# Kernel optimization log

Measured on AMD Instinct MI355X. Metric: run time of the kernel, lower is better.

Reference implementation:

```python
import jax, jax.numpy as jnp
import numpy as np

N, D = 4096, 128
NUM_CLASS = 500000
NUM_SAMPLES = 32768


def setup_inputs() -> dict:
    key = jax.random.key(0)
    k_x, k_w, k_b, k_id = jax.random.split(key, 4)
    x = jax.random.normal(k_x, (N, D), dtype=jnp.float32)
    # params.weight init uniform(-0.05, 0.05) in original; use randn-scaled equivalent scale
    weight = jax.random.normal(k_w, (NUM_CLASS, D), dtype=jnp.float32) * 0.05
    bias = jax.random.normal(k_b, (NUM_CLASS, 1), dtype=jnp.float32) * 0.01
    # sample_ids: candidate classes returned by the LSH hash-table query (host-side
    # data structure); modeled here as a precomputed index set.
    sample_ids = jax.random.randint(k_id, (NUM_SAMPLES,), 0, NUM_CLASS, dtype=jnp.int64)
    return {"x": x, "weight": weight, "bias": bias, "sample_ids": sample_ids}


def reference(x, weight, bias, sample_ids):
    # gather sampled class embeddings + biases (F.embedding equivalent)
    sample_weights = weight[sample_ids]            # [S, D]
    sample_bias = bias[:, 0][sample_ids]           # [S]
    # small GEMM: [N, D] @ [D, S] + [S]
    sample_logits = jnp.einsum("nd,sd->ns", x, sample_weights) + sample_bias
    return (sample_logits, sample_ids)
```

## Files before the change

### kernel.cpp

```cpp
#include <hip/hip_runtime.h>

#define NROWS 4096
#define DIM   128
#define SCOLS 32768

typedef short bf16x8 __attribute__((ext_vector_type(8)));
typedef float f32x4  __attribute__((ext_vector_type(4)));

__device__ __forceinline__ unsigned short f2bf(float f) {
    unsigned int u = __builtin_bit_cast(unsigned int, f);
    u += 0x7fffu + ((u >> 16) & 1u);
    return (unsigned short)(u >> 16);
}

#define WCHUNKS (SCOLS * 16)
#define XCHUNKS (NROWS * 16)

__global__ __launch_bounds__(256) void prep_kernel(
    const float* __restrict__ x, const float* __restrict__ weight,
    const float* __restrict__ bias, const int* __restrict__ ids,
    float* __restrict__ out, unsigned short* __restrict__ w_ws,
    unsigned short* __restrict__ x_ws, float* __restrict__ bias_ws)
{
    int gid = blockIdx.x * 256 + threadIdx.x;
    if (gid < WCHUNKS) {
        int r = gid >> 4, c = gid & 15;
        int id = ids[r];
        const float4* src = (const float4*)(weight + (size_t)id * DIM);
        float4 v0 = src[2 * c], v1 = src[2 * c + 1];
        union { unsigned short u[8]; uint4 q; } b;
        b.u[0] = f2bf(v0.x); b.u[1] = f2bf(v0.y); b.u[2] = f2bf(v0.z); b.u[3] = f2bf(v0.w);
        b.u[4] = f2bf(v1.x); b.u[5] = f2bf(v1.y); b.u[6] = f2bf(v1.z); b.u[7] = f2bf(v1.w);
        *(uint4*)&w_ws[(size_t)r * DIM + (size_t)((c ^ (r & 15)) * 8)] = b.q;
    } else if (gid < WCHUNKS + XCHUNKS) {
        int g = gid - WCHUNKS;
        int r = g >> 4, c = g & 15;
        const float4* src = (const float4*)(x + (size_t)r * DIM);
        float4 v0 = src[2 * c], v1 = src[2 * c + 1];
        union { unsigned short u[8]; uint4 q; } b;
        b.u[0] = f2bf(v0.x); b.u[1] = f2bf(v0.y); b.u[2] = f2bf(v0.z); b.u[3] = f2bf(v0.w);
        b.u[4] = f2bf(v1.x); b.u[5] = f2bf(v1.y); b.u[6] = f2bf(v1.z); b.u[7] = f2bf(v1.w);
        *(uint4*)&x_ws[(size_t)r * DIM + (size_t)((c ^ (r & 15)) * 8)] = b.q;
    } else {
        int g = gid - (WCHUNKS + XCHUNKS);
        if (g < SCOLS) {
            int id = ids[g];
            bias_ws[g] = bias[id];
            out[(size_t)NROWS * SCOLS + g] = (float)id;
        }
    }
}

__global__ __launch_bounds__(256, 2) void lsh_gemm2(
    const unsigned short* __restrict__ w_ws,
    const unsigned short* __restrict__ x_ws,
    const float* __restrict__ bias_ws,
    float* __restrict__ out)
{
    __shared__ unsigned short lds_w[128 * 128];
    __shared__ unsigned short lds_x[128 * 128];

    const int t    = threadIdx.x;
    const int s0   = blockIdx.x * 128;
    const int n0   = blockIdx.y * 128;
    const int lane = t & 63;
    const int wave = t >> 6;

    const char* wsrc = (const char*)(w_ws + (size_t)s0 * DIM);
    const char* xsrc = (const char*)(x_ws + (size_t)n0 * DIM);

    #pragma unroll
    for (int j = 0; j < 8; ++j) {
        int boff = wave * 8192 + j * 1024;
        int goff = boff + lane * 16;
        __builtin_amdgcn_global_load_lds(
            (const __attribute__((address_space(1))) void*)(wsrc + goff),
            (__attribute__((address_space(3))) void*)((char*)lds_w + boff),
            16, 0, 0);
        __builtin_amdgcn_global_load_lds(
            (const __attribute__((address_space(1))) void*)(xsrc + goff),
            (__attribute__((address_space(3))) void*)((char*)lds_x + boff),
            16, 0, 0);
    }
    __syncthreads();

    const int lrow = lane & 15;
    const int quad = lane >> 4;
    const int wn   = (wave & 1) * 64;
    const int wsc  = (wave >> 1) * 64;

    f32x4 acc[4][4];
    #pragma unroll
    for (int a = 0; a < 4; ++a)
        #pragma unroll
        for (int b = 0; b < 4; ++b)
            acc[a][b] = (f32x4){0.f, 0.f, 0.f, 0.f};

    #pragma unroll
    for (int kk = 0; kk < 4; ++kk) {
        bf16x8 aw[4], bx[4];
        int cb = kk * 4 + quad;
        #pragma unroll
        for (int i = 0; i < 4; ++i) {
            int rw = wsc + i * 16 + lrow;
            int rn = wn  + i * 16 + lrow;
            aw[i] = *(const bf16x8*)&lds_w[rw * 128 + ((cb ^ lrow) * 8)];
            bx[i] = *(const bf16x8*)&lds_x[rn * 128 + ((cb ^ lrow) * 8)];
        }
        #pragma unroll
        for (int a = 0; a < 4; ++a)
            #pragma unroll
            for (int b = 0; b < 4; ++b)
                acc[a][b] = __builtin_amdgcn_mfma_f32_16x16x32_bf16(
                    aw[a], bx[b], acc[a][b], 0, 0, 0);
    }

    #pragma unroll
    for (int a = 0; a < 4; ++a) {
        int sL = wsc + a * 16 + quad * 4;
        f32x4 b4 = *(const f32x4*)&bias_ws[s0 + sL];
        #pragma unroll
        for (int b = 0; b < 4; ++b) {
            int n = n0 + wn + b * 16 + lrow;
            f32x4 v = acc[a][b] + b4;
            __builtin_nontemporal_store(v, (f32x4*)&out[(size_t)n * SCOLS + (s0 + sL)]);
        }
    }
}

__global__ __launch_bounds__(256, 2) void lsh_gemm(
    const float* __restrict__ x,
    const float* __restrict__ weight,
    const float* __restrict__ bias,
    const int*   __restrict__ ids,
    float*       __restrict__ out)
{
    __shared__ unsigned short lds_x[128 * 128];
    __shared__ unsigned short lds_w[128 * 128];

    const int t  = threadIdx.x;
    const int s0 = blockIdx.x * 128;
    const int n0 = blockIdx.y * 128;

    #pragma unroll
    for (int i = 0; i < 16; ++i) {
        int f   = t + i * 256;
        int row = f >> 5;
        int c4  = f & 31;
        float4 v = ((const float4*)(x + (size_t)(n0 + row) * DIM))[c4];
        ushort4 b;
        b.x = f2bf(v.x); b.y = f2bf(v.y); b.z = f2bf(v.z); b.w = f2bf(v.w);
        int sw = (c4 >> 1) ^ (row & 15);
        *(ushort4*)&lds_x[row * 128 + sw * 8 + (c4 & 1) * 4] = b;
    }
    #pragma unroll
    for (int i = 0; i < 16; ++i) {
        int f   = t + i * 256;
        int row = f >> 5;
        int c4  = f & 31;
        int id  = ids[s0 + row];
        float4 v = ((const float4*)(weight + (size_t)id * DIM))[c4];
        ushort4 b;
        b.x = f2bf(v.x); b.y = f2bf(v.y); b.z = f2bf(v.z); b.w = f2bf(v.w);
        int sw = (c4 >> 1) ^ (row & 15);
        *(ushort4*)&lds_w[row * 128 + sw * 8 + (c4 & 1) * 4] = b;
    }
    __syncthreads();

    const int lane = t & 63;
    const int wave = t >> 6;
    const int lrow = lane & 15;
    const int quad = lane >> 4;
    const int wm   = (wave & 1) * 64;
    const int wsc  = (wave >> 1) * 64;

    f32x4 acc[4][4];
    #pragma unroll
    for (int a = 0; a < 4; ++a)
        #pragma unroll
        for (int b = 0; b < 4; ++b)
            acc[a][b] = (f32x4){0.f, 0.f, 0.f, 0.f};

    #pragma unroll
    for (int kk = 0; kk < 4; ++kk) {
        bf16x8 af[4], bv[4];
        int cbase = kk * 4 + quad;
        #pragma unroll
        for (int i = 0; i < 4; ++i) {
            int rowa = wm  + i * 16 + lrow;
            int rowb = wsc + i * 16 + lrow;
            af[i] = *(const bf16x8*)&lds_x[rowa * 128 + (cbase ^ lrow) * 8];
            bv[i] = *(const bf16x8*)&lds_w[rowb * 128 + (cbase ^ lrow) * 8];
        }
        #pragma unroll
        for (int tm = 0; tm < 4; ++tm)
            #pragma unroll
            for (int ts = 0; ts < 4; ++ts)
                acc[tm][ts] = __builtin_amdgcn_mfma_f32_16x16x32_bf16(
                    af[tm], bv[ts], acc[tm][ts], 0, 0, 0);
    }

    #pragma unroll
    for (int ts = 0; ts < 4; ++ts) {
        int colL = wsc + ts * 16 + lrow;
        int col  = s0 + colL;
        float bvps = bias[ids[s0 + colL]];
        #pragma unroll
        for (int tm = 0; tm < 4; ++tm) {
            int rowbase = n0 + wm + tm * 16 + quad * 4;
            #pragma unroll
            for (int r = 0; r < 4; ++r)
                out[(size_t)(rowbase + r) * SCOLS + col] = acc[tm][ts][r] + bvps;
        }
    }
}

__global__ void ids_out_kernel(const int* __restrict__ ids, float* __restrict__ out)
{
    int i = blockIdx.x * 256 + threadIdx.x;
    if (i < SCOLS)
        out[(size_t)NROWS * SCOLS + i] = (float)ids[i];
}

extern "C" void kernel_launch(void* const* d_in, const int* in_sizes, int n_in,
                              void* d_out, int out_size, void* d_ws, size_t ws_size,
                              hipStream_t stream) {
    const float* x      = (const float*)d_in[0];
    const float* weight = (const float*)d_in[1];
    const float* bias   = (const float*)d_in[2];
    const int*   ids    = (const int*)d_in[3];
    float*       out    = (float*)d_out;

    const size_t W_BYTES = (size_t)SCOLS * DIM * 2;
    const size_t X_BYTES = (size_t)NROWS * DIM * 2;
    const size_t B_BYTES = (size_t)SCOLS * 4;

    if (ws_size >= W_BYTES + X_BYTES + B_BYTES) {
        unsigned short* w_ws   = (unsigned short*)d_ws;
        unsigned short* x_ws   = (unsigned short*)((char*)d_ws + W_BYTES);
        float*          bias_ws = (float*)((char*)d_ws + W_BYTES + X_BYTES);

        const int prep_blocks = (WCHUNKS + XCHUNKS + SCOLS) / 256;
        hipLaunchKernelGGL(prep_kernel, dim3(prep_blocks), dim3(256), 0, stream,
                           x, weight, bias, ids, out, w_ws, x_ws, bias_ws);
        hipLaunchKernelGGL(lsh_gemm2, dim3(SCOLS / 128, NROWS / 128), dim3(256), 0, stream,
                           w_ws, x_ws, bias_ws, out);
    } else {
        hipLaunchKernelGGL(lsh_gemm, dim3(SCOLS / 128, NROWS / 128), dim3(256), 0, stream,
                           x, weight, bias, ids, out);
        hipLaunchKernelGGL(ids_out_kernel, dim3(SCOLS / 256), dim3(256), 0, stream,
                           ids, out);
    }
}
```

Measured before the change: 660.7 us.

## Make GEMM blocks sweep multiple column tiles reusing resident x tile

Replaces the 2D grid of single-tile blocks with 512 blocks, each keeping its 128-row x tile in LDS and looping over 16 consecutive weight tiles. Each iteration computes, stores with bias, then reloads the next W tile into LDS between barriers. This is meant to cut redundant x loads and block launch/scheduling overhead. The trade-off is that the W reload is serialized with compute, with no double buffering, and the fixed 512-block grid can suffer load imbalance.

```diff
diff --git a/kernel.cpp b/kernel.cpp
--- a/kernel.cpp
+++ b/kernel.cpp
@@ -51,7 +51,9 @@
     }
 }
 
-__global__ __launch_bounds__(256, 2) void lsh_gemm2(
+#define SWEEP 16
+
+__global__ __launch_bounds__(256, 2) void lsh_gemm3(
     const unsigned short* __restrict__ w_ws,
     const unsigned short* __restrict__ x_ws,
     const float* __restrict__ bias_ws,
@@ -61,26 +63,24 @@
     __shared__ unsigned short lds_x[128 * 128];
 
     const int t    = threadIdx.x;
-    const int s0   = blockIdx.x * 128;
-    const int n0   = blockIdx.y * 128;
     const int lane = t & 63;
     const int wave = t >> 6;
-
-    const char* wsrc = (const char*)(w_ws + (size_t)s0 * DIM);
+    const int nt   = blockIdx.x >> 4;
+    const int sc   = blockIdx.x & 15;
+    const int n0   = nt * 128;
+
     const char* xsrc = (const char*)(x_ws + (size_t)n0 * DIM);
-
-    #pragma unroll
-    for (int j = 0; j < 8; ++j) {
-        int boff = wave * 8192 + j * 1024;
-        int goff = boff + lane * 16;
+    const char* wchunk = (const char*)(w_ws + (size_t)(sc * SWEEP) * 128 * DIM);
+
+    #pragma unroll
+    for (int jj = 0; jj < 8; ++jj) {
+        int boff = wave * 8192 + jj * 1024;
         __builtin_amdgcn_global_load_lds(
-            (const __attribute__((address_space(1))) void*)(wsrc + goff),
-            (__attribute__((address_space(3))) void*)((char*)lds_w + boff),
-            16, 0, 0);
+            (const __attribute__((address_space(1))) void*)(xsrc + boff + lane * 16),
+            (__attribute__((address_space(3))) void*)((char*)lds_x + boff), 16, 0, 0);
         __builtin_amdgcn_global_load_lds(
-            (const __attribute__((address_space(1))) void*)(xsrc + goff),
-            (__attribute__((address_space(3))) void*)((char*)lds_x + boff),
-            16, 0, 0);
+            (const __attribute__((address_space(1))) void*)(wchunk + boff + lane * 16),
+            (__attribute__((address_space(3))) void*)((char*)lds_w + boff), 16, 0, 0);
     }
     __syncthreads();
 
@@ -89,41 +89,58 @@
     const int wn   = (wave & 1) * 64;
     const int wsc  = (wave >> 1) * 64;
 
-    f32x4 acc[4][4];
-    #pragma unroll
-    for (int a = 0; a < 4; ++a)
-        #pragma unroll
-        for (int b = 0; b < 4; ++b)
-            acc[a][b] = (f32x4){0.f, 0.f, 0.f, 0.f};
-
-    #pragma unroll
-    for (int kk = 0; kk < 4; ++kk) {
-        bf16x8 aw[4], bx[4];
-        int cb = kk * 4 + quad;
-        #pragma unroll
-        for (int i = 0; i < 4; ++i) {
-            int rw = wsc + i * 16 + lrow;
-            int rn = wn  + i * 16 + lrow;
-            aw[i] = *(const bf16x8*)&lds_w[rw * 128 + ((cb ^ lrow) * 8)];
-            bx[i] = *(const bf16x8*)&lds_x[rn * 128 + ((cb ^ lrow) * 8)];
-        }
+    for (int j = 0; j < SWEEP; ++j) {
+        const int s0 = (sc * SWEEP + j) * 128;
+
+        f32x4 acc[4][4];
         #pragma unroll
         for (int a = 0; a < 4; ++a)
             #pragma unroll
             for (int b = 0; b < 4; ++b)
-                acc[a][b] = __builtin_amdgcn_mfma_f32_16x16x32_bf16(
-                    aw[a], bx[b], acc[a][b], 0, 0, 0);
-    }
-
-    #pragma unroll
-    for (int a = 0; a < 4; ++a) {
-        int sL = wsc + a * 16 + quad * 4;
-        f32x4 b4 = *(const f32x4*)&bias_ws[s0 + sL];
-        #pragma unroll
-        for (int b = 0; b < 4; ++b) {
-            int n = n0 + wn + b * 16 + lrow;
-            f32x4 v = acc[a][b] + b4;
-            __builtin_nontemporal_store(v, (f32x4*)&out[(size_t)n * SCOLS + (s0 + sL)]);
+                acc[a][b] = (f32x4){0.f, 0.f, 0.f, 0.f};
+
+        #pragma unroll
+        for (int kk = 0; kk < 4; ++kk) {
+            bf16x8 aw[4], bx[4];
+            int cb = kk * 4 + quad;
+            #pragma unroll
+            for (int i = 0; i < 4; ++i) {
+                int rw = wsc + i * 16 + lrow;
+                int rn = wn  + i * 16 + lrow;
+                aw[i] = *(const bf16x8*)&lds_w[rw * 128 + ((cb ^ lrow) * 8)];
+                bx[i] = *(const bf16x8*)&lds_x[rn * 128 + ((cb ^ lrow) * 8)];
+            }
+            #pragma unroll
+            for (int a = 0; a < 4; ++a)
+                #pragma unroll
+                for (int b = 0; b < 4; ++b)
+                    acc[a][b] = __builtin_amdgcn_mfma_f32_16x16x32_bf16(
+                        aw[a], bx[b], acc[a][b], 0, 0, 0);
+        }
+
+        #pragma unroll
+        for (int a = 0; a < 4; ++a) {
+            int sL = wsc + a * 16 + quad * 4;
+            f32x4 b4 = *(const f32x4*)&bias_ws[s0 + sL];
+            #pragma unroll
+            for (int b = 0; b < 4; ++b) {
+                int n = n0 + wn + b * 16 + lrow;
+                f32x4 v = acc[a][b] + b4;
+                __builtin_nontemporal_store(v, (f32x4*)&out[(size_t)n * SCOLS + (s0 + sL)]);
+            }
+        }
+
+        if (j + 1 < SWEEP) {
+            __syncthreads();
+            const char* wsrc = wchunk + (size_t)(j + 1) * 128 * DIM * 2;
+            #pragma unroll
+            for (int jj = 0; jj < 8; ++jj) {
+                int boff = wave * 8192 + jj * 1024;
+                __builtin_amdgcn_global_load_lds(
+                    (const __attribute__((address_space(1))) void*)(wsrc + boff + lane * 16),
+                    (__attribute__((address_space(3))) void*)((char*)lds_w + boff), 16, 0, 0);
+            }
+            __syncthreads();
         }
     }
 }
@@ -236,14 +253,14 @@
     const size_t B_BYTES = (size_t)SCOLS * 4;
 
     if (ws_size >= W_BYTES + X_BYTES + B_BYTES) {
-        unsigned short* w_ws   = (unsigned short*)d_ws;
-        unsigned short* x_ws   = (unsigned short*)((char*)d_ws + W_BYTES);
+        unsigned short* w_ws    = (unsigned short*)d_ws;
+        unsigned short* x_ws    = (unsigned short*)((char*)d_ws + W_BYTES);
         float*          bias_ws = (float*)((char*)d_ws + W_BYTES + X_BYTES);
 
         const int prep_blocks = (WCHUNKS + XCHUNKS + SCOLS) / 256;
         hipLaunchKernelGGL(prep_kernel, dim3(prep_blocks), dim3(256), 0, stream,
                            x, weight, bias, ids, out, w_ws, x_ws, bias_ws);
-        hipLaunchKernelGGL(lsh_gemm2, dim3(SCOLS / 128, NROWS / 128), dim3(256), 0, stream,
+        hipLaunchKernelGGL(lsh_gemm3, dim3(512), dim3(256), 0, stream,
                            w_ws, x_ws, bias_ws, out);
     } else {
         hipLaunchKernelGGL(lsh_gemm, dim3(SCOLS / 128, NROWS / 128), dim3(256), 0, stream,
```

New measurement: 770.3 us. 16.6% more time.
